# Kernel tuning notes

Measured on AMD Instinct MI355X. Metric: run time of the kernel, lower is better.

The kernel has to match this reference:

```python
import jax, jax.numpy as jnp
import numpy as np

B = 2          # graphs (images)
GRID = 13      # patches per spatial dim -> N = 169 patches per image
N = GRID * GRID
NN = B * N     # total nodes
C = 256        # hidden_dim / out_channels per head
H = 4          # attention heads
L = 3          # GAT layers
LRELU_SLOPE = 0.2
LN_EPS = 1e-5


def _dense_edges():
    # fully-connected directed graph (i != j) per image, as in create_graph
    idx = np.arange(N)
    src, dst = np.meshgrid(idx, idx, indexing='ij')
    mask = src != dst
    src, dst = src[mask], dst[mask]              # [N*(N-1)]
    offs = (np.arange(B) * N)[:, None]
    e_src = (src[None, :] + offs).reshape(-1)
    e_dst = (dst[None, :] + offs).reshape(-1)
    return e_src.astype(np.int32), e_dst.astype(np.int32)


def setup_inputs() -> dict:
    key = jax.random.key(0)
    ks = jax.random.split(key, 8)
    s = 0.05
    e_src, e_dst = _dense_edges()
    return {
        'x':   jax.random.normal(ks[0], (NN, C), jnp.float32),
        'Wl':  jax.random.normal(ks[1], (L, C, H * C), jnp.float32) * s,
        'bl':  jnp.zeros((L, H * C), jnp.float32),
        'Wr':  jax.random.normal(ks[2], (L, C, H * C), jnp.float32) * s,
        'br':  jnp.zeros((L, H * C), jnp.float32),
        'att': jax.random.normal(ks[3], (L, H, C), jnp.float32) * s,
        'bias': jnp.zeros((L, C), jnp.float32),
        'ln_g': jnp.ones((L, C), jnp.float32),
        'ln_b': jnp.zeros((L, C), jnp.float32),
        'W1':  jax.random.normal(ks[4], (L, C, 2 * C), jnp.float32) * s,
        'b1':  jnp.zeros((L, 2 * C), jnp.float32),
        'W2':  jax.random.normal(ks[5], (L, 2 * C, C), jnp.float32) * s,
        'b2':  jnp.zeros((L, C), jnp.float32),
        'edge_src': jnp.asarray(e_src),
        'edge_dst': jnp.asarray(e_dst),
        'batch_ids': jnp.repeat(jnp.arange(B, dtype=jnp.int32), N),
    }


def _gatv2(x, Wl, bl, Wr, br, att, bias, src, dst, n_nodes):
    # PyG GATv2Conv, concat=False (mean over heads)
    xl = (x @ Wl + bl).reshape(n_nodes, H, C)   # source transform
    xr = (x @ Wr + br).reshape(n_nodes, H, C)   # target transform
    e = jax.nn.leaky_relu(xl[src] + xr[dst], LRELU_SLOPE)     # [E,H,C]
    logits = jnp.einsum('ehc,hc->eh', e, att)                 # [E,H]
    m = jax.ops.segment_max(logits, dst, num_segments=n_nodes)
    a = jnp.exp(logits - m[dst])
    z = jax.ops.segment_sum(a, dst, num_segments=n_nodes)
    alpha = a / (z[dst] + 1e-16)                              # softmax per target
    msg = alpha[:, :, None] * xl[src]                         # [E,H,C]
    agg = jax.ops.segment_sum(msg, dst, num_segments=n_nodes) # [N,H,C]
    return agg.mean(axis=1) + bias


def _layernorm(x, g, b):
    mu = x.mean(-1, keepdims=True)
    var = jnp.mean((x - mu) ** 2, -1, keepdims=True)
    return (x - mu) * jax.lax.rsqrt(var + LN_EPS) * g + b


def reference(x, Wl, bl, Wr, br, att, bias, ln_g, ln_b, W1, b1, W2, b2,
              edge_src, edge_dst, batch_ids):
    n_nodes = x.shape[0]
    for l in range(L):
        residual = x
        h = _gatv2(x, Wl[l], bl[l], Wr[l], br[l], att[l], bias[l],
                   edge_src, edge_dst, n_nodes)
        h = _layernorm(h, ln_g[l], ln_b[l])
        mlp = jnp.maximum(h @ W1[l] + b1[l], 0.0) @ W2[l] + b2[l]
        x = residual + mlp
    # global mean pool per graph
    sums = jax.ops.segment_sum(x, batch_ids, num_segments=B)
    cnts = jax.ops.segment_sum(jnp.ones((n_nodes, 1), x.dtype), batch_ids,
                               num_segments=B)
    return sums / cnts
```

## Files before the change

### kernel.cpp

```cpp
#include <hip/hip_runtime.h>
#include <hip/hip_bf16.h>

typedef __hip_bfloat16 bf16;

#define NNODES 169
#define NNTOT  338
#define CH     256
#define NH     4
#define NL     3
#define SPAD   176
#define LN_EPS 1e-5f

__device__ __forceinline__ float b2f(bf16 v) { return __bfloat162float(v); }
__device__ __forceinline__ float lrelu(float v) { return fmaxf(v, 0.2f * v); }
__device__ __forceinline__ float ldm(const void* p, size_t i, int isbf) {
    return isbf ? b2f(((const bf16*)p)[i]) : ((const float*)p)[i];
}
__device__ __forceinline__ int sniff_bf(const void* lng) {
    return ((((const unsigned*)lng)[0] & 0xFFFFu) == 0x3F80u) ? 1 : 0;
}

__global__ __launch_bounds__(256) void k_gemm_lr(
    const void* __restrict__ Av, int israw,
    const void* __restrict__ Wl, const void* __restrict__ bl,
    const void* __restrict__ Wr, const void* __restrict__ br,
    size_t oW, size_t oB,
    float* __restrict__ xl, float* __restrict__ xr, float* __restrict__ xlT,
    const void* __restrict__ lng)
{
    __shared__ float As[32 * 36];
    __shared__ float Ws[32 * 64];
    const int isbf  = sniff_bf(lng);
    const int a_bf  = israw ? isbf : 0;
    const int wr    = (blockIdx.z != 0);
    const void* Wv  = wr ? Wr : Wl;
    const void* bv_ = wr ? br : bl;
    float* out      = wr ? xr : xl;

    const int tid  = threadIdx.x;
    const int row0 = blockIdx.x * 32, col0 = blockIdx.y * 64;
    const int c0 = (tid & 15) * 4;
    const int r0 = (tid >> 4) * 2;
    const int ar = tid >> 3;
    const int ak = (tid & 7) * 4;
    const int wk = tid >> 3;
    const int wn = (tid & 7) * 8;
    const int K = CH, N = NH * CH, M = NNTOT;

    float acc[2][4] = {{0.f,0.f,0.f,0.f},{0.f,0.f,0.f,0.f}};

    for (int k0 = 0; k0 < K; k0 += 32) {
        float4 av = make_float4(0.f, 0.f, 0.f, 0.f);
        const int gr = row0 + ar;
        if (gr < M) {
            const size_t ai = (size_t)gr * K + k0 + ak;
            if (israw) {
                av.x = ldm(Av, ai + 0, a_bf); av.y = ldm(Av, ai + 1, a_bf);
                av.z = ldm(Av, ai + 2, a_bf); av.w = ldm(Av, ai + 3, a_bf);
            } else {
                av = *(const float4*)((const float*)Av + ai);
            }
        }
        float wv8[8];
        const size_t widx = oW + (size_t)(k0 + wk) * N + col0 + wn;
        if (isbf) {
            const int4 wi = *(const int4*)((const bf16*)Wv + widx);
            union { unsigned u; float f; } t;
            t.u = ((unsigned)wi.x) << 16;         wv8[0] = t.f;
            t.u = ((unsigned)wi.x) & 0xFFFF0000u; wv8[1] = t.f;
            t.u = ((unsigned)wi.y) << 16;         wv8[2] = t.f;
            t.u = ((unsigned)wi.y) & 0xFFFF0000u; wv8[3] = t.f;
            t.u = ((unsigned)wi.z) << 16;         wv8[4] = t.f;
            t.u = ((unsigned)wi.z) & 0xFFFF0000u; wv8[5] = t.f;
            t.u = ((unsigned)wi.w) << 16;         wv8[6] = t.f;
            t.u = ((unsigned)wi.w) & 0xFFFF0000u; wv8[7] = t.f;
        } else {
            const float* Wf = (const float*)Wv;
            const float4 w0 = *(const float4*)(Wf + widx);
            const float4 w1 = *(const float4*)(Wf + widx + 4);
            wv8[0] = w0.x; wv8[1] = w0.y; wv8[2] = w0.z; wv8[3] = w0.w;
            wv8[4] = w1.x; wv8[5] = w1.y; wv8[6] = w1.z; wv8[7] = w1.w;
        }
        __syncthreads();
        As[ar * 36 + ak + 0] = av.x; As[ar * 36 + ak + 1] = av.y;
        As[ar * 36 + ak + 2] = av.z; As[ar * 36 + ak + 3] = av.w;
        #pragma unroll
        for (int j = 0; j < 8; j++) Ws[wk * 64 + wn + j] = wv8[j];
        __syncthreads();
        #pragma unroll
        for (int k = 0; k < 32; k++) {
            const float a0 = As[r0 * 36 + k];
            const float a1 = As[(r0 + 1) * 36 + k];
            const float4 wv = *(const float4*)&Ws[k * 64 + c0];
            acc[0][0] += a0 * wv.x; acc[0][1] += a0 * wv.y;
            acc[0][2] += a0 * wv.z; acc[0][3] += a0 * wv.w;
            acc[1][0] += a1 * wv.x; acc[1][1] += a1 * wv.y;
            acc[1][2] += a1 * wv.z; acc[1][3] += a1 * wv.w;
        }
    }

    float bvv[4];
    #pragma unroll
    for (int j = 0; j < 4; j++) bvv[j] = ldm(bv_, oB + col0 + c0 + j, isbf);
    #pragma unroll
    for (int i = 0; i < 2; i++) {
        const int gr = row0 + r0 + i;
        if (gr >= M) continue;
        float4 v;
        v.x = acc[i][0] + bvv[0]; v.y = acc[i][1] + bvv[1];
        v.z = acc[i][2] + bvv[2]; v.w = acc[i][3] + bvv[3];
        *(float4*)(out + (size_t)gr * N + col0 + c0) = v;
        if (!wr) {
            const int col = col0 + c0;
            const int hh = col >> 8, cc = col & 255;
            const int gg = (gr >= NNODES) ? 1 : 0;
            const int ss = gr - gg * NNODES;
            float* tb = xlT + ((size_t)(gg * NH + hh) * CH + cc) * SPAD + ss;
            tb[0] = v.x; tb[SPAD] = v.y; tb[2 * SPAD] = v.z; tb[3 * SPAD] = v.w;
        }
    }
}

__global__ __launch_bounds__(192) void k_logits_sm(
    const float* __restrict__ xlT, const float* __restrict__ xr,
    const void* __restrict__ att, size_t oA,
    float* __restrict__ alphaR, const void* __restrict__ lng)
{
    __shared__ float s_att[CH];
    __shared__ float s_xr[2 * CH];
    __shared__ float s_tile[32 * SPAD];
    __shared__ float s_log[2 * SPAD];
    const int isbf = sniff_bf(lng);
    const int g = blockIdx.z, h = blockIdx.y, d0 = blockIdx.x * 2;
    const int tid = threadIdx.x, lane = tid & 63, wv = tid >> 6;

    for (int idx = tid; idx < CH; idx += 192)
        s_att[idx] = ldm(att, oA + h * CH + idx, isbf);
    for (int idx = tid; idx < 2 * CH; idx += 192) {
        const int i = idx >> 8, c = idx & 255, d = d0 + i;
        s_xr[idx] = (d < NNODES)
            ? xr[(size_t)(g * NNODES + d) * (NH * CH) + h * CH + c] : 0.f;
    }

    float l0 = 0.f, l1 = 0.f;
    const int s = tid;
    const float4* src = (const float4*)(xlT + ((size_t)(g * NH + h) * CH) * SPAD);
    for (int ch = 0; ch < 8; ch++) {
        __syncthreads();
        #pragma unroll 2
        for (int i = tid; i < 32 * SPAD / 4; i += 192)
            ((float4*)s_tile)[i] = src[ch * (32 * SPAD / 4) + i];
        __syncthreads();
        if (s < NNODES) {
            const int cb = ch * 32;
            #pragma unroll
            for (int c = 0; c < 32; c++) {
                const float v = s_tile[c * SPAD + s];
                const float a = s_att[cb + c];
                l0 += a * lrelu(v + s_xr[cb + c]);
                l1 += a * lrelu(v + s_xr[CH + cb + c]);
            }
        }
    }
    if (s < NNODES) { s_log[s] = l0; s_log[SPAD + s] = l1; }
    __syncthreads();

    if (wv < 2) {
        const int d = d0 + wv;
        const float* row = s_log + wv * SPAD;
        const int s0 = lane, s1 = lane + 64, s2 = lane + 128;
        const float v0 = (s0 < NNODES && s0 != d) ? row[s0] : -1e30f;
        const float v1 = (s1 < NNODES && s1 != d) ? row[s1] : -1e30f;
        const float v2 = (s2 < NNODES && s2 != d) ? row[s2] : -1e30f;
        float mx = fmaxf(v0, fmaxf(v1, v2));
        mx = fmaxf(mx, __shfl_xor(mx, 32)); mx = fmaxf(mx, __shfl_xor(mx, 16));
        mx = fmaxf(mx, __shfl_xor(mx, 8));  mx = fmaxf(mx, __shfl_xor(mx, 4));
        mx = fmaxf(mx, __shfl_xor(mx, 2));  mx = fmaxf(mx, __shfl_xor(mx, 1));
        const float e0 = expf(v0 - mx), e1 = expf(v1 - mx), e2 = expf(v2 - mx);
        float z = e0 + e1 + e2;
        z += __shfl_xor(z, 32); z += __shfl_xor(z, 16); z += __shfl_xor(z, 8);
        z += __shfl_xor(z, 4);  z += __shfl_xor(z, 2);  z += __shfl_xor(z, 1);
        const float sc = 0.25f / (z + 1e-16f);
        if (d < NNODES) {
            float* arow = alphaR + ((size_t)(g * NH + h) * NNODES + d) * SPAD;
            if (s0 < NNODES) arow[s0] = e0 * sc;
            if (s1 < NNODES) arow[s1] = e1 * sc;
            if (s2 < NNODES) arow[s2] = e2 * sc;
        }
    }
}

__global__ __launch_bounds__(256) void k_agg(
    const float* __restrict__ alphaR, const float* __restrict__ xl,
    float* __restrict__ part)
{
    __shared__ float s_a[32 * 33];
    __shared__ float s_x[32 * 64];
    const int gh = blockIdx.z, g = gh >> 2, h = gh & 3;
    const int d0 = blockIdx.x * 32, c0 = blockIdx.y * 64;
    const int tid = threadIdx.x;
    const int dr = (tid >> 4) * 2, cq = (tid & 15) * 4;
    const int sr = tid >> 3, sc4 = (tid & 7) * 4;
    const int xc8 = (tid & 7) * 8;

    float acc[2][4] = {{0.f,0.f,0.f,0.f},{0.f,0.f,0.f,0.f}};

    for (int s0 = 0; s0 < NNODES; s0 += 32) {
        __syncthreads();
        {
            const int d = d0 + sr;
            const float* ap = alphaR + ((size_t)gh * NNODES + d) * SPAD + s0 + sc4;
            const int ok = (d < NNODES);
            s_a[sr * 33 + sc4 + 0] = (ok && s0 + sc4 + 0 < NNODES) ? ap[0] : 0.f;
            s_a[sr * 33 + sc4 + 1] = (ok && s0 + sc4 + 1 < NNODES) ? ap[1] : 0.f;
            s_a[sr * 33 + sc4 + 2] = (ok && s0 + sc4 + 2 < NNODES) ? ap[2] : 0.f;
            s_a[sr * 33 + sc4 + 3] = (ok && s0 + sc4 + 3 < NNODES) ? ap[3] : 0.f;
        }
        {
            const int sg = s0 + sr;
            if (sg < NNODES) {
                const float* xp = xl + (size_t)(g * NNODES + sg) * (NH * CH) + h * CH + c0 + xc8;
                *(float4*)&s_x[sr * 64 + xc8]     = *(const float4*)(xp);
                *(float4*)&s_x[sr * 64 + xc8 + 4] = *(const float4*)(xp + 4);
            } else {
                #pragma unroll
                for (int j = 0; j < 8; j++) s_x[sr * 64 + xc8 + j] = 0.f;
            }
        }
        __syncthreads();
        #pragma unroll
        for (int k = 0; k < 32; k++) {
            const float a0 = s_a[(dr + 0) * 33 + k];
            const float a1 = s_a[(dr + 1) * 33 + k];
            const float4 xv = *(const float4*)&s_x[k * 64 + cq];
            acc[0][0] += a0 * xv.x; acc[0][1] += a0 * xv.y;
            acc[0][2] += a0 * xv.z; acc[0][3] += a0 * xv.w;
            acc[1][0] += a1 * xv.x; acc[1][1] += a1 * xv.y;
            acc[1][2] += a1 * xv.z; acc[1][3] += a1 * xv.w;
        }
    }
    #pragma unroll
    for (int i = 0; i < 2; i++) {
        const int d = d0 + dr + i;
        if (d >= NNODES) continue;
        float4 v;
        v.x = acc[i][0]; v.y = acc[i][1]; v.z = acc[i][2]; v.w = acc[i][3];
        *(float4*)(part + ((size_t)h * NNTOT + g * NNODES + d) * CH + c0 + cq) = v;
    }
}

__global__ __launch_bounds__(256) void k_ln(
    const float* __restrict__ part,
    const void* __restrict__ bias, size_t oB,
    const void* __restrict__ ln_g, size_t oG,
    const void* __restrict__ ln_b, size_t oBt,
    float* __restrict__ h_out, const void* __restrict__ lng)
{
    __shared__ float s_red[8];
    const int isbf = sniff_bf(lng);
    const int node = blockIdx.x, c = threadIdx.x;
    const int lane = c & 63, wv = c >> 6;

    float vch = part[((size_t)0 * NNTOT + node) * CH + c]
              + part[((size_t)1 * NNTOT + node) * CH + c]
              + part[((size_t)2 * NNTOT + node) * CH + c]
              + part[((size_t)3 * NNTOT + node) * CH + c]
              + ldm(bias, oB + c, isbf);

    float s1 = vch, s2 = vch * vch;
    s1 += __shfl_xor(s1, 32); s2 += __shfl_xor(s2, 32);
    s1 += __shfl_xor(s1, 16); s2 += __shfl_xor(s2, 16);
    s1 += __shfl_xor(s1, 8);  s2 += __shfl_xor(s2, 8);
    s1 += __shfl_xor(s1, 4);  s2 += __shfl_xor(s2, 4);
    s1 += __shfl_xor(s1, 2);  s2 += __shfl_xor(s2, 2);
    s1 += __shfl_xor(s1, 1);  s2 += __shfl_xor(s2, 1);
    if (lane == 0) { s_red[wv] = s1; s_red[4 + wv] = s2; }
    __syncthreads();
    const float S1 = s_red[0] + s_red[1] + s_red[2] + s_red[3];
    const float S2 = s_red[4] + s_red[5] + s_red[6] + s_red[7];
    const float mu  = S1 * (1.f / CH);
    const float var = S2 * (1.f / CH) - mu * mu;
    const float o = (vch - mu) * rsqrtf(var + LN_EPS) * ldm(ln_g, oG + c, isbf)
                  + ldm(ln_b, oBt + c, isbf);
    h_out[(size_t)node * CH + c] = o;
}

__global__ __launch_bounds__(256) void k_mlp1(
    const float* __restrict__ A, const void* __restrict__ W, size_t oW,
    const void* __restrict__ b, size_t oB,
    float* __restrict__ out, const void* __restrict__ lng)
{
    __shared__ float As[32 * 36];
    __shared__ float Ws[32 * 32];
    const int isbf = sniff_bf(lng);
    const int tid = threadIdx.x;
    const int row0 = blockIdx.x * 32, col0 = blockIdx.y * 32;
    const int row = tid >> 3, c4 = (tid & 7) * 4;
    const int K = CH, N = 2 * CH, M = NNTOT;

    float acc[4] = {0.f, 0.f, 0.f, 0.f};

    for (int k0 = 0; k0 < K; k0 += 32) {
        float4 av = make_float4(0.f, 0.f, 0.f, 0.f);
        const int gr = row0 + row;
        if (gr < M) av = *(const float4*)(A + (size_t)gr * K + k0 + c4);
        float wv4[4];
        const size_t widx = oW + (size_t)(k0 + row) * N + col0 + c4;
        if (isbf) {
            const int2 wi = *(const int2*)((const bf16*)W + widx);
            union { unsigned u; float f; } t;
            t.u = ((unsigned)wi.x) << 16;         wv4[0] = t.f;
            t.u = ((unsigned)wi.x) & 0xFFFF0000u; wv4[1] = t.f;
            t.u = ((unsigned)wi.y) << 16;         wv4[2] = t.f;
            t.u = ((unsigned)wi.y) & 0xFFFF0000u; wv4[3] = t.f;
        } else {
            const float4 w0 = *(const float4*)((const float*)W + widx);
            wv4[0] = w0.x; wv4[1] = w0.y; wv4[2] = w0.z; wv4[3] = w0.w;
        }
        __syncthreads();
        As[row * 36 + c4 + 0] = av.x; As[row * 36 + c4 + 1] = av.y;
        As[row * 36 + c4 + 2] = av.z; As[row * 36 + c4 + 3] = av.w;
        #pragma unroll
        for (int j = 0; j < 4; j++) Ws[row * 32 + c4 + j] = wv4[j];
        __syncthreads();
        #pragma unroll
        for (int k = 0; k < 32; k++) {
            const float a = As[row * 36 + k];
            const float4 wv = *(const float4*)&Ws[k * 32 + c4];
            acc[0] += a * wv.x; acc[1] += a * wv.y;
            acc[2] += a * wv.z; acc[3] += a * wv.w;
        }
    }
    const int gr = row0 + row;
    if (gr < M) {
        float4 v;
        v.x = fmaxf(acc[0] + ldm(b, oB + col0 + c4 + 0, isbf), 0.f);
        v.y = fmaxf(acc[1] + ldm(b, oB + col0 + c4 + 1, isbf), 0.f);
        v.z = fmaxf(acc[2] + ldm(b, oB + col0 + c4 + 2, isbf), 0.f);
        v.w = fmaxf(acc[3] + ldm(b, oB + col0 + c4 + 3, isbf), 0.f);
        *(float4*)(out + (size_t)gr * N + col0 + c4) = v;
    }
}

__global__ __launch_bounds__(256) void k_mlp2(
    const float* __restrict__ A, const void* __restrict__ W, size_t oW,
    const void* __restrict__ b, size_t oB,
    const void* __restrict__ x_res, int israw,
    float* __restrict__ out, const void* __restrict__ lng)
{
    __shared__ float As[16 * 34];
    __shared__ float Ws[32 * 32];
    const int isbf = sniff_bf(lng);
    const int r_bf = israw ? isbf : 0;
    const int tid = threadIdx.x;
    const int row0 = blockIdx.x * 16, col0 = blockIdx.y * 32;
    const int row = tid >> 4, c2 = (tid & 15) * 2;
    const int wk = tid >> 3, wc4 = (tid & 7) * 4;
    const int K = 2 * CH, N = CH, M = NNTOT;

    float acc[2] = {0.f, 0.f};

    for (int k0 = 0; k0 < K; k0 += 32) {
        float2 av = make_float2(0.f, 0.f);
        const int gr = row0 + row;
        if (gr < M) av = *(const float2*)(A + (size_t)gr * K + k0 + c2);
        float wv4[4];
        const size_t widx = oW + (size_t)(k0 + wk) * N + col0 + wc4;
        if (isbf) {
            const int2 wi = *(const int2*)((const bf16*)W + widx);
            union { unsigned u; float f; } t;
            t.u = ((unsigned)wi.x) << 16;         wv4[0] = t.f;
            t.u = ((unsigned)wi.x) & 0xFFFF0000u; wv4[1] = t.f;
            t.u = ((unsigned)wi.y) << 16;         wv4[2] = t.f;
            t.u = ((unsigned)wi.y) & 0xFFFF0000u; wv4[3] = t.f;
        } else {
            const float4 w0 = *(const float4*)((const float*)W + widx);
            wv4[0] = w0.x; wv4[1] = w0.y; wv4[2] = w0.z; wv4[3] = w0.w;
        }
        __syncthreads();
        As[row * 34 + c2 + 0] = av.x; As[row * 34 + c2 + 1] = av.y;
        #pragma unroll
        for (int j = 0; j < 4; j++) Ws[wk * 32 + wc4 + j] = wv4[j];
        __syncthreads();
        #pragma unroll
        for (int k = 0; k < 32; k++) {
            const float a = As[row * 34 + k];
            const float2 wv = *(const float2*)&Ws[k * 32 + c2];
            acc[0] += a * wv.x; acc[1] += a * wv.y;
        }
    }
    const int gr = row0 + row;
    if (gr < M) {
        const size_t ro = (size_t)gr * N + col0 + c2;
        const float o0 = acc[0] + ldm(b, oB + col0 + c2 + 0, isbf) + ldm(x_res, ro, r_bf);
        const float o1 = acc[1] + ldm(b, oB + col0 + c2 + 1, isbf) + ldm(x_res, ro + 1, r_bf);
        out[ro]     = o0;
        out[ro + 1] = o1;
    }
}

__global__ __launch_bounds__(256) void k_pool(const float* __restrict__ x,
                                              void* __restrict__ out,
                                              const void* __restrict__ lng) {
    const int isbf = sniff_bf(lng);
    const int g = blockIdx.x, c = threadIdx.x;
    float s = 0.f;
    const float* p = x + (size_t)g * NNODES * CH + c;
    for (int n = 0; n < NNODES; n++) s += p[(size_t)n * CH];
    const float v = s * (1.f / NNODES);
    if (isbf) ((bf16*)out)[g * CH + c] = __float2bfloat16(v);
    else      ((float*)out)[g * CH + c] = v;
}

extern "C" void kernel_launch(void* const* d_in, const int* in_sizes, int n_in,
                              void* d_out, int out_size, void* d_ws, size_t ws_size,
                              hipStream_t stream)
{
    const void* x_in = d_in[0];
    const void* Wl   = d_in[1];
    const void* bl   = d_in[2];
    const void* Wr   = d_in[3];
    const void* br   = d_in[4];
    const void* att  = d_in[5];
    const void* bias = d_in[6];
    const void* lng  = d_in[7];
    const void* lnb  = d_in[8];
    const void* W1   = d_in[9];
    const void* b1   = d_in[10];
    const void* W2   = d_in[11];
    const void* b2   = d_in[12];

    float* ws     = (float*)d_ws;
    float* xl     = ws;
    float* xr     = xl + (size_t)NNTOT * NH * CH;
    float* xlT    = xr + (size_t)NNTOT * NH * CH;
    float* alphaR = xlT + (size_t)2 * NH * CH * SPAD;
    float* part   = alphaR + (size_t)2 * NH * NNODES * SPAD;
    float* h_ln   = part + (size_t)NH * NNTOT * CH;
    float* m1     = h_ln + (size_t)NNTOT * CH;
    float* xa     = m1 + (size_t)NNTOT * 2 * CH;
    float* xb     = xa + (size_t)NNTOT * CH;

    const size_t sW  = (size_t)CH * NH * CH;
    const size_t sB  = NH * CH;
    const size_t sA  = NH * CH;
    const size_t sC  = CH;
    const size_t sW1 = (size_t)CH * 2 * CH;
    const size_t sB1 = 2 * CH;
    const size_t sW2 = (size_t)2 * CH * CH;

    const void* x_l[3] = { x_in, xa, xb };
    float*      x_o[3] = { xa, xb, xa };

    for (int l = 0; l < NL; l++) {
        const int israw = (l == 0);
        k_gemm_lr<<<dim3(11, 16, 2), 256, 0, stream>>>(
            x_l[l], israw, Wl, bl, Wr, br,
            (size_t)l * sW, (size_t)l * sB, xl, xr, xlT, lng);
        k_logits_sm<<<dim3(85, NH, 2), 192, 0, stream>>>(
            xlT, xr, att, (size_t)l * sA, alphaR, lng);
        k_agg<<<dim3(6, 4, 8), 256, 0, stream>>>(alphaR, xl, part);
        k_ln<<<dim3(NNTOT), 256, 0, stream>>>(
            part, bias, (size_t)l * sC, lng, (size_t)l * sC, lnb, (size_t)l * sC,
            h_ln, lng);
        k_mlp1<<<dim3(11, 16), 256, 0, stream>>>(
            h_ln, W1, (size_t)l * sW1, b1, (size_t)l * sB1, m1, lng);
        k_mlp2<<<dim3(22, 8), 256, 0, stream>>>(
            m1, W2, (size_t)l * sW2, b2, (size_t)l * sC,
            x_l[l], israw, x_o[l], lng);
    }

    k_pool<<<dim3(2), 256, 0, stream>>>(xa, d_out, lng);
}
```

Before: 322.6 us.

## Replace scalar FP32 GEMMs with split-bf16 MFMA GEMM and weight pre-transpose

Result: no change. 327.7 us (+1.6%).

```diff
diff --git a/kernel.cpp b/kernel.cpp
--- a/kernel.cpp
+++ b/kernel.cpp
@@ -2,6 +2,10 @@
 #include <hip/hip_bf16.h>
 
 typedef __hip_bfloat16 bf16;
+typedef __attribute__((ext_vector_type(4))) float f32x4;
+typedef __attribute__((ext_vector_type(8))) unsigned short u16x8;
+typedef __attribute__((ext_vector_type(4))) unsigned short u16x4;
+typedef __bf16 bf16x8 __attribute__((ext_vector_type(8)));
 
 #define NNODES 169
 #define NNTOT  338
@@ -19,104 +23,183 @@
 __device__ __forceinline__ int sniff_bf(const void* lng) {
     return ((((const unsigned*)lng)[0] & 0xFFFFu) == 0x3F80u) ? 1 : 0;
 }
-
-__global__ __launch_bounds__(256) void k_gemm_lr(
-    const void* __restrict__ Av, int israw,
-    const void* __restrict__ Wl, const void* __restrict__ bl,
-    const void* __restrict__ Wr, const void* __restrict__ br,
-    size_t oW, size_t oB,
-    float* __restrict__ xl, float* __restrict__ xr, float* __restrict__ xlT,
+__device__ __forceinline__ unsigned short f2bf_rn(float f) {
+    unsigned u = __float_as_uint(f);
+    u += 0x7FFFu + ((u >> 16) & 1u);
+    return (unsigned short)(u >> 16);
+}
+__device__ __forceinline__ float bfb2f(unsigned short h) {
+    return __uint_as_float(((unsigned)h) << 16);
+}
+
+__global__ __launch_bounds__(256) void k_wprep(
+    const void* __restrict__ Wl, const void* __restrict__ Wr,
+    const void* __restrict__ W1, const void* __restrict__ W2,
+    unsigned short* __restrict__ wlT, unsigned short* __restrict__ wrT,
+    unsigned short* __restrict__ w1T, unsigned short* __restrict__ w2T,
     const void* __restrict__ lng)
 {
-    __shared__ float As[32 * 36];
-    __shared__ float Ws[32 * 64];
-    const int isbf  = sniff_bf(lng);
-    const int a_bf  = israw ? isbf : 0;
-    const int wr    = (blockIdx.z != 0);
-    const void* Wv  = wr ? Wr : Wl;
-    const void* bv_ = wr ? br : bl;
-    float* out      = wr ? xr : xl;
-
-    const int tid  = threadIdx.x;
-    const int row0 = blockIdx.x * 32, col0 = blockIdx.y * 64;
-    const int c0 = (tid & 15) * 4;
-    const int r0 = (tid >> 4) * 2;
-    const int ar = tid >> 3;
-    const int ak = (tid & 7) * 4;
-    const int wk = tid >> 3;
-    const int wn = (tid & 7) * 8;
-    const int K = CH, N = NH * CH, M = NNTOT;
-
-    float acc[2][4] = {{0.f,0.f,0.f,0.f},{0.f,0.f,0.f,0.f}};
+    __shared__ unsigned short sH[64 * 72];
+    __shared__ unsigned short sL[64 * 72];
+    const int isbf = sniff_bf(lng);
+    int t = blockIdx.x;
+    const void* src; unsigned short* dst; int K, N;
+    if (t < 384)      { K = 256; N = 1024; src = (t < 192) ? Wl : Wr;
+                        dst = (t < 192) ? wlT : wrT; t = t % 192; }
+    else if (t < 480) { K = 256; N = 512;  src = W1; dst = w1T; t -= 384; }
+    else              { K = 512; N = 256;  src = W2; dst = w2T; t -= 480; }
+    const int ntiles = N / 64;
+    const int tpl = (K / 64) * ntiles;
+    const int l = t / tpl; t %= tpl;
+    const int k0 = (t / ntiles) * 64, n0 = (t % ntiles) * 64;
+    const size_t loPlane = (size_t)NL * K * N;
+    const int tid = threadIdx.x;
+
+    const int kk = tid >> 2, q = tid & 3;
+    if (isbf) {
+        const bf16* srow = (const bf16*)src + ((size_t)l * K + k0 + kk) * N + n0;
+        #pragma unroll
+        for (int i = 0; i < 4; i++) {
+            const int c = q * 4 + i * 16;
+            const int2 w = *(const int2*)(srow + c);
+            const unsigned short u0 = (unsigned short)(w.x & 0xFFFF);
+            const unsigned short u1 = (unsigned short)(((unsigned)w.x) >> 16);
+            const unsigned short u2 = (unsigned short)(w.y & 0xFFFF);
+            const unsigned short u3 = (unsigned short)(((unsigned)w.y) >> 16);
+            sH[kk * 72 + c + 0] = u0; sL[kk * 72 + c + 0] = 0;
+            sH[kk * 72 + c + 1] = u1; sL[kk * 72 + c + 1] = 0;
+            sH[kk * 72 + c + 2] = u2; sL[kk * 72 + c + 2] = 0;
+            sH[kk * 72 + c + 3] = u3; sL[kk * 72 + c + 3] = 0;
+        }
+    } else {
+        const float* srow = (const float*)src + ((size_t)l * K + k0 + kk) * N + n0;
+        #pragma unroll
+        for (int i = 0; i < 4; i++) {
+            const int c = q * 4 + i * 16;
+            const float4 v4 = *(const float4*)(srow + c);
+            const float vv[4] = { v4.x, v4.y, v4.z, v4.w };
+            #pragma unroll
+            for (int j = 0; j < 4; j++) {
+                const unsigned short h = f2bf_rn(vv[j]);
+                sH[kk * 72 + c + j] = h;
+                sL[kk * 72 + c + j] = f2bf_rn(vv[j] - bfb2f(h));
+            }
+        }
+    }
+    __syncthreads();
+    for (int u = tid; u < 512; u += 256) {
+        const int n = u >> 3, k8 = (u & 7) * 8;
+        u16x8 hh, ll;
+        #pragma unroll
+        for (int j = 0; j < 8; j++) {
+            hh[j] = sH[(k8 + j) * 72 + n];
+            ll[j] = sL[(k8 + j) * 72 + n];
+        }
+        unsigned short* dh = dst + ((size_t)l * N + n0 + n) * K + k0 + k8;
+        *(u16x8*)dh = hh;
+        *(u16x8*)(dh + loPlane) = ll;
+    }
+}
+
+__global__ __launch_bounds__(256) void k_gemm_mfma(
+    const void* __restrict__ A, int a_raw, int K, int N,
+    const unsigned short* __restrict__ wH0, const unsigned short* __restrict__ wL0,
+    const unsigned short* __restrict__ wH1, const unsigned short* __restrict__ wL1,
+    const void* __restrict__ bias0, const void* __restrict__ bias1, size_t oB,
+    const void* __restrict__ res, int r_raw,
+    float* __restrict__ out0, float* __restrict__ out1,
+    float* __restrict__ xlT, int mode, const void* __restrict__ lng)
+{
+    __shared__ unsigned short sAh[32 * 40], sAl[32 * 40];
+    __shared__ unsigned short sBh[64 * 40], sBl[64 * 40];
+    const int isbf = sniff_bf(lng);
+    const int z = blockIdx.z;
+    const unsigned short* wH = z ? wH1 : wH0;
+    const unsigned short* wL = z ? wL1 : wL0;
+    const void* bias = z ? bias1 : bias0;
+    float* out = z ? out1 : out0;
+    const int a_bf = a_raw ? isbf : 0;
+    const int tid = threadIdx.x;
+    const int wave = tid >> 6, lane = tid & 63, l15 = lane & 15, g = lane >> 4;
+    const int m0 = blockIdx.x * 32, n0 = blockIdx.y * 64;
+
+    const int ar = tid >> 3, ak = (tid & 7) * 4;
+    const int bn = tid >> 2, boct = tid & 3;
+
+    f32x4 acc0 = {0.f, 0.f, 0.f, 0.f};
+    f32x4 acc1 = {0.f, 0.f, 0.f, 0.f};
+    const float* Af = (const float*)A;
 
     for (int k0 = 0; k0 < K; k0 += 32) {
-        float4 av = make_float4(0.f, 0.f, 0.f, 0.f);
-        const int gr = row0 + ar;
-        if (gr < M) {
-            const size_t ai = (size_t)gr * K + k0 + ak;
-            if (israw) {
-                av.x = ldm(Av, ai + 0, a_bf); av.y = ldm(Av, ai + 1, a_bf);
-                av.z = ldm(Av, ai + 2, a_bf); av.w = ldm(Av, ai + 3, a_bf);
-            } else {
-                av = *(const float4*)((const float*)Av + ai);
+        unsigned short h4[4] = {0, 0, 0, 0}, l4[4] = {0, 0, 0, 0};
+        {
+            const int grow = m0 + ar;
+            if (grow < NNTOT) {
+                const size_t ai = (size_t)grow * K + k0 + ak;
+                if (a_bf) {
+                    const int2 w = *(const int2*)((const bf16*)A + ai);
+                    h4[0] = (unsigned short)(w.x & 0xFFFF);
+                    h4[1] = (unsigned short)(((unsigned)w.x) >> 16);
+                    h4[2] = (unsigned short)(w.y & 0xFFFF);
+                    h4[3] = (unsigned short)(((unsigned)w.y) >> 16);
+                } else {
+                    const float4 t = *(const float4*)(Af + ai);
+                    const float vv[4] = { t.x, t.y, t.z, t.w };
+                    #pragma unroll
+                    for (int j = 0; j < 4; j++) {
+                        h4[j] = f2bf_rn(vv[j]);
+                        l4[j] = f2bf_rn(vv[j] - bfb2f(h4[j]));
+                    }
+                }
             }
         }
-        float wv8[8];
-        const size_t widx = oW + (size_t)(k0 + wk) * N + col0 + wn;
-        if (isbf) {
-            const int4 wi = *(const int4*)((const bf16*)Wv + widx);
-            union { unsigned u; float f; } t;
-            t.u = ((unsigned)wi.x) << 16;         wv8[0] = t.f;
-            t.u = ((unsigned)wi.x) & 0xFFFF0000u; wv8[1] = t.f;
-            t.u = ((unsigned)wi.y) << 16;         wv8[2] = t.f;
-            t.u = ((unsigned)wi.y) & 0xFFFF0000u; wv8[3] = t.f;
-            t.u = ((unsigned)wi.z) << 16;         wv8[4] = t.f;
-            t.u = ((unsigned)wi.z) & 0xFFFF0000u; wv8[5] = t.f;
-            t.u = ((unsigned)wi.w) << 16;         wv8[6] = t.f;
-            t.u = ((unsigned)wi.w) & 0xFFFF0000u; wv8[7] = t.f;
-        } else {
-            const float* Wf = (const float*)Wv;
-            const float4 w0 = *(const float4*)(Wf + widx);
-            const float4 w1 = *(const float4*)(Wf + widx + 4);
-            wv8[0] = w0.x; wv8[1] = w0.y; wv8[2] = w0.z; wv8[3] = w0.w;
-            wv8[4] = w1.x; wv8[5] = w1.y; wv8[6] = w1.z; wv8[7] = w1.w;
-        }
-        __syncthreads();
-        As[ar * 36 + ak + 0] = av.x; As[ar * 36 + ak + 1] = av.y;
-        As[ar * 36 + ak + 2] = av.z; As[ar * 36 + ak + 3] = av.w;
+        const size_t bi = (size_t)(n0 + bn) * K + k0 + boct * 8;
+        const u16x8 bhv = *(const u16x8*)(wH + bi);
+        const u16x8 blv = *(const u16x8*)(wL + bi);
+        __syncthreads();
+        {
+            u16x4 ha, la;
+            ha[0] = h4[0]; ha[1] = h4[1]; ha[2] = h4[2]; ha[3] = h4[3];
+            la[0] = l4[0]; la[1] = l4[1]; la[2] = l4[2]; la[3] = l4[3];
+            *(u16x4*)&sAh[ar * 40 + ak] = ha;
+            *(u16x4*)&sAl[ar * 40 + ak] = la;
+            *(u16x8*)&sBh[bn * 40 + boct * 8] = bhv;
+            *(u16x8*)&sBl[bn * 40 + boct * 8] = blv;
+        }
+        __syncthreads();
+        const bf16x8 a_h0 = *(const bf16x8*)&sAh[l15 * 40 + g * 8];
+        const bf16x8 a_h1 = *(const bf16x8*)&sAh[(16 + l15) * 40 + g * 8];
+        const bf16x8 a_l0 = *(const bf16x8*)&sAl[l15 * 40 + g * 8];
+        const bf16x8 a_l1 = *(const bf16x8*)&sAl[(16 + l15) * 40 + g * 8];
+        const bf16x8 b_h  = *(const bf16x8*)&sBh[(wave * 16 + l15) * 40 + g * 8];
+        const bf16x8 b_l  = *(const bf16x8*)&sBl[(wave * 16 + l15) * 40 + g * 8];
+        acc0 = __builtin_amdgcn_mfma_f32_16x16x32_bf16(a_h0, b_h, acc0, 0, 0, 0);
+        acc1 = __builtin_amdgcn_mfma_f32_16x16x32_bf16(a_h1, b_h, acc1, 0, 0, 0);
+        acc0 = __builtin_amdgcn_mfma_f32_16x16x32_bf16(a_l0, b_h, acc0, 0, 0, 0);
+        acc1 = __builtin_amdgcn_mfma_f32_16x16x32_bf16(a_l1, b_h, acc1, 0, 0, 0);
+        acc0 = __builtin_amdgcn_mfma_f32_16x16x32_bf16(a_h0, b_l, acc0, 0, 0, 0);
+        acc1 = __builtin_amdgcn_mfma_f32_16x16x32_bf16(a_h1, b_l, acc1, 0, 0, 0);
+    }
+
+    const int col = n0 + wave * 16 + l15;
+    const float bv = ldm(bias, oB + col, isbf);
+    #pragma unroll
+    for (int mi = 0; mi < 2; mi++) {
+        const f32x4 a = mi ? acc1 : acc0;
         #pragma unroll
-        for (int j = 0; j < 8; j++) Ws[wk * 64 + wn + j] = wv8[j];
-        __syncthreads();
-        #pragma unroll
-        for (int k = 0; k < 32; k++) {
-            const float a0 = As[r0 * 36 + k];
-            const float a1 = As[(r0 + 1) * 36 + k];
-            const float4 wv = *(const float4*)&Ws[k * 64 + c0];
-            acc[0][0] += a0 * wv.x; acc[0][1] += a0 * wv.y;
-            acc[0][2] += a0 * wv.z; acc[0][3] += a0 * wv.w;
-            acc[1][0] += a1 * wv.x; acc[1][1] += a1 * wv.y;
-            acc[1][2] += a1 * wv.z; acc[1][3] += a1 * wv.w;
-        }
-    }
-
-    float bvv[4];
-    #pragma unroll
-    for (int j = 0; j < 4; j++) bvv[j] = ldm(bv_, oB + col0 + c0 + j, isbf);
-    #pragma unroll
-    for (int i = 0; i < 2; i++) {
-        const int gr = row0 + r0 + i;
-        if (gr >= M) continue;
-        float4 v;
-        v.x = acc[i][0] + bvv[0]; v.y = acc[i][1] + bvv[1];
-        v.z = acc[i][2] + bvv[2]; v.w = acc[i][3] + bvv[3];
-        *(float4*)(out + (size_t)gr * N + col0 + c0) = v;
-        if (!wr) {
-            const int col = col0 + c0;
-            const int hh = col >> 8, cc = col & 255;
-            const int gg = (gr >= NNODES) ? 1 : 0;
-            const int ss = gr - gg * NNODES;
-            float* tb = xlT + ((size_t)(gg * NH + hh) * CH + cc) * SPAD + ss;
-            tb[0] = v.x; tb[SPAD] = v.y; tb[2 * SPAD] = v.z; tb[3 * SPAD] = v.w;
+        for (int r = 0; r < 4; r++) {
+            const int row = m0 + mi * 16 + g * 4 + r;
+            if (row >= NNTOT) continue;
+            float v = a[r] + bv;
+            if (mode == 1) v = fmaxf(v, 0.f);
+            if (mode == 2) v += ldm(res, (size_t)row * N + col, r_raw ? isbf : 0);
+            out[(size_t)row * N + col] = v;
+            if (mode == 0 && z == 0) {
+                const int hh = col >> 8, cc = col & 255;
+                const int gg = (row >= NNODES) ? 1 : 0;
+                const int ss = row - gg * NNODES;
+                xlT[((size_t)(gg * NH + hh) * CH + cc) * SPAD + ss] = v;
+            }
         }
     }
 }
@@ -177,10 +260,10 @@
         mx = fmaxf(mx, __shfl_xor(mx, 8));  mx = fmaxf(mx, __shfl_xor(mx, 4));
         mx = fmaxf(mx, __shfl_xor(mx, 2));  mx = fmaxf(mx, __shfl_xor(mx, 1));
         const float e0 = expf(v0 - mx), e1 = expf(v1 - mx), e2 = expf(v2 - mx);
-        float z = e0 + e1 + e2;
-        z += __shfl_xor(z, 32); z += __shfl_xor(z, 16); z += __shfl_xor(z, 8);
-        z += __shfl_xor(z, 4);  z += __shfl_xor(z, 2);  z += __shfl_xor(z, 1);
-        const float sc = 0.25f / (z + 1e-16f);
+        float zz = e0 + e1 + e2;
+        zz += __shfl_xor(zz, 32); zz += __shfl_xor(zz, 16); zz += __shfl_xor(zz, 8);
+        zz += __shfl_xor(zz, 4);  zz += __shfl_xor(zz, 2);  zz += __shfl_xor(zz, 1);
+        const float sc = 0.25f / (zz + 1e-16f);
         if (d < NNODES) {
             float* arow = alphaR + ((size_t)(g * NH + h) * NNODES + d) * SPAD;
             if (s0 < NNODES) arow[s0] = e0 * sc;
@@ -285,120 +368,6 @@
     h_out[(size_t)node * CH + c] = o;
 }
 
-__global__ __launch_bounds__(256) void k_mlp1(
-    const float* __restrict__ A, const void* __restrict__ W, size_t oW,
-    const void* __restrict__ b, size_t oB,
-    float* __restrict__ out, const void* __restrict__ lng)
-{
-    __shared__ float As[32 * 36];
-    __shared__ float Ws[32 * 32];
-    const int isbf = sniff_bf(lng);
-    const int tid = threadIdx.x;
-    const int row0 = blockIdx.x * 32, col0 = blockIdx.y * 32;
-    const int row = tid >> 3, c4 = (tid & 7) * 4;
-    const int K = CH, N = 2 * CH, M = NNTOT;
-
-    float acc[4] = {0.f, 0.f, 0.f, 0.f};
-
-    for (int k0 = 0; k0 < K; k0 += 32) {
-        float4 av = make_float4(0.f, 0.f, 0.f, 0.f);
-        const int gr = row0 + row;
-        if (gr < M) av = *(const float4*)(A + (size_t)gr * K + k0 + c4);
-        float wv4[4];
-        const size_t widx = oW + (size_t)(k0 + row) * N + col0 + c4;
-        if (isbf) {
-            const int2 wi = *(const int2*)((const bf16*)W + widx);
-            union { unsigned u; float f; } t;
-            t.u = ((unsigned)wi.x) << 16;         wv4[0] = t.f;
-            t.u = ((unsigned)wi.x) & 0xFFFF0000u; wv4[1] = t.f;
-            t.u = ((unsigned)wi.y) << 16;         wv4[2] = t.f;
-            t.u = ((unsigned)wi.y) & 0xFFFF0000u; wv4[3] = t.f;
-        } else {
-            const float4 w0 = *(const float4*)((const float*)W + widx);
-            wv4[0] = w0.x; wv4[1] = w0.y; wv4[2] = w0.z; wv4[3] = w0.w;
-        }
-        __syncthreads();
-        As[row * 36 + c4 + 0] = av.x; As[row * 36 + c4 + 1] = av.y;
-        As[row * 36 + c4 + 2] = av.z; As[row * 36 + c4 + 3] = av.w;
-        #pragma unroll
-        for (int j = 0; j < 4; j++) Ws[row * 32 + c4 + j] = wv4[j];
-        __syncthreads();
-        #pragma unroll
-        for (int k = 0; k < 32; k++) {
-            const float a = As[row * 36 + k];
-            const float4 wv = *(const float4*)&Ws[k * 32 + c4];
-            acc[0] += a * wv.x; acc[1] += a * wv.y;
-            acc[2] += a * wv.z; acc[3] += a * wv.w;
-        }
-    }
-    const int gr = row0 + row;
-    if (gr < M) {
-        float4 v;
-        v.x = fmaxf(acc[0] + ldm(b, oB + col0 + c4 + 0, isbf), 0.f);
-        v.y = fmaxf(acc[1] + ldm(b, oB + col0 + c4 + 1, isbf), 0.f);
-        v.z = fmaxf(acc[2] + ldm(b, oB + col0 + c4 + 2, isbf), 0.f);
-        v.w = fmaxf(acc[3] + ldm(b, oB + col0 + c4 + 3, isbf), 0.f);
-        *(float4*)(out + (size_t)gr * N + col0 + c4) = v;
-    }
-}
-
-__global__ __launch_bounds__(256) void k_mlp2(
-    const float* __restrict__ A, const void* __restrict__ W, size_t oW,
-    const void* __restrict__ b, size_t oB,
-    const void* __restrict__ x_res, int israw,
-    float* __restrict__ out, const void* __restrict__ lng)
-{
-    __shared__ float As[16 * 34];
-    __shared__ float Ws[32 * 32];
-    const int isbf = sniff_bf(lng);
-    const int r_bf = israw ? isbf : 0;
-    const int tid = threadIdx.x;
-    const int row0 = blockIdx.x * 16, col0 = blockIdx.y * 32;
-    const int row = tid >> 4, c2 = (tid & 15) * 2;
-    const int wk = tid >> 3, wc4 = (tid & 7) * 4;
-    const int K = 2 * CH, N = CH, M = NNTOT;
-
-    float acc[2] = {0.f, 0.f};
-
-    for (int k0 = 0; k0 < K; k0 += 32) {
-        float2 av = make_float2(0.f, 0.f);
-        const int gr = row0 + row;
-        if (gr < M) av = *(const float2*)(A + (size_t)gr * K + k0 + c2);
-        float wv4[4];
-        const size_t widx = oW + (size_t)(k0 + wk) * N + col0 + wc4;
-        if (isbf) {
-            const int2 wi = *(const int2*)((const bf16*)W + widx);
-            union { unsigned u; float f; } t;
-            t.u = ((unsigned)wi.x) << 16;         wv4[0] = t.f;
-            t.u = ((unsigned)wi.x) & 0xFFFF0000u; wv4[1] = t.f;
-            t.u = ((unsigned)wi.y) << 16;         wv4[2] = t.f;
-            t.u = ((unsigned)wi.y) & 0xFFFF0000u; wv4[3] = t.f;
-        } else {
-            const float4 w0 = *(const float4*)((const float*)W + widx);
-            wv4[0] = w0.x; wv4[1] = w0.y; wv4[2] = w0.z; wv4[3] = w0.w;
-        }
-        __syncthreads();
-        As[row * 34 + c2 + 0] = av.x; As[row * 34 + c2 + 1] = av.y;
-        #pragma unroll
-        for (int j = 0; j < 4; j++) Ws[wk * 32 + wc4 + j] = wv4[j];
-        __syncthreads();
-        #pragma unroll
-        for (int k = 0; k < 32; k++) {
-            const float a = As[row * 34 + k];
-            const float2 wv = *(const float2*)&Ws[k * 32 + c2];
-            acc[0] += a * wv.x; acc[1] += a * wv.y;
-        }
-    }
-    const int gr = row0 + row;
-    if (gr < M) {
-        const size_t ro = (size_t)gr * N + col0 + c2;
-        const float o0 = acc[0] + ldm(b, oB + col0 + c2 + 0, isbf) + ldm(x_res, ro, r_bf);
-        const float o1 = acc[1] + ldm(b, oB + col0 + c2 + 1, isbf) + ldm(x_res, ro + 1, r_bf);
-        out[ro]     = o0;
-        out[ro + 1] = o1;
-    }
-}
-
 __global__ __launch_bounds__(256) void k_pool(const float* __restrict__ x,
                                               void* __restrict__ out,
                                               const void* __restrict__ lng) {
@@ -441,33 +410,54 @@
     float* xa     = m1 + (size_t)NNTOT * 2 * CH;
     float* xb     = xa + (size_t)NNTOT * CH;
 
-    const size_t sW  = (size_t)CH * NH * CH;
+    unsigned short* wbt = (unsigned short*)(xb + (size_t)NNTOT * CH);
+    const size_t pLR = (size_t)NL * (NH * CH) * CH;
+    const size_t pM  = (size_t)NL * (2 * CH) * CH;
+    unsigned short* wlT = wbt;
+    unsigned short* wrT = wlT + 2 * pLR;
+    unsigned short* w1T = wrT + 2 * pLR;
+    unsigned short* w2T = w1T + 2 * pM;
+    const size_t lyLR = (size_t)(NH * CH) * CH;
+    const size_t lyM  = (size_t)(2 * CH) * CH;
+
     const size_t sB  = NH * CH;
-    const size_t sA  = NH * CH;
     const size_t sC  = CH;
-    const size_t sW1 = (size_t)CH * 2 * CH;
     const size_t sB1 = 2 * CH;
-    const size_t sW2 = (size_t)2 * CH * CH;
 
     const void* x_l[3] = { x_in, xa, xb };
     float*      x_o[3] = { xa, xb, xa };
 
+    k_wprep<<<dim3(576), 256, 0, stream>>>(Wl, Wr, W1, W2, wlT, wrT, w1T, w2T, lng);
+
     for (int l = 0; l < NL; l++) {
         const int israw = (l == 0);
-        k_gemm_lr<<<dim3(11, 16, 2), 256, 0, stream>>>(
-            x_l[l], israw, Wl, bl, Wr, br,
-            (size_t)l * sW, (size_t)l * sB, xl, xr, xlT, lng);
+        k_gemm_mfma<<<dim3(11, 16, 2), 256, 0, stream>>>(
+            x_l[l], israw, CH, NH * CH,
+            wlT + l * lyLR, wlT + pLR + l * lyLR,
+            wrT + l * lyLR, wrT + pLR + l * lyLR,
+            bl, br, (size_t)l * sB,
+            nullptr, 0,
+            xl, xr, xlT, 0, lng);
         k_logits_sm<<<dim3(85, NH, 2), 192, 0, stream>>>(
-            xlT, xr, att, (size_t)l * sA, alphaR, lng);
+            xlT, xr, att, (size_t)l * sB, alphaR, lng);
         k_agg<<<dim3(6, 4, 8), 256, 0, stream>>>(alphaR, xl, part);
         k_ln<<<dim3(NNTOT), 256, 0, stream>>>(
             part, bias, (size_t)l * sC, lng, (size_t)l * sC, lnb, (size_t)l * sC,
             h_ln, lng);
-        k_mlp1<<<dim3(11, 16), 256, 0, stream>>>(
-            h_ln, W1, (size_t)l * sW1, b1, (size_t)l * sB1, m1, lng);
-        k_mlp2<<<dim3(22, 8), 256, 0, stream>>>(
-            m1, W2, (size_t)l * sW2, b2, (size_t)l * sC,
-            x_l[l], israw, x_o[l], lng);
+        k_gemm_mfma<<<dim3(11, 8, 1), 256, 0, stream>>>(
+            h_ln, 0, CH, 2 * CH,
+            w1T + l * lyM, w1T + pM + l * lyM,
+            w1T + l * lyM, w1T + pM + l * lyM,
+            b1, b1, (size_t)l * sB1,
+            nullptr, 0,
+            m1, m1, nullptr, 1, lng);
+        k_gemm_mfma<<<dim3(11, 4, 1), 256, 0, stream>>>(
+            m1, 0, 2 * CH, CH,
+            w2T + l * lyM, w2T + pM + l * lyM,
+            w2T + l * lyM, w2T + pM + l * lyM,
+            b2, b2, (size_t)l * sC,
+            x_l[l], israw,
+            x_o[l], x_o[l], nullptr, 2, lng);
     }
 
     k_pool<<<dim3(2), 256, 0, stream>>>(xa, d_out, lng);
```
